# Optimization experiments

Hardware: AMD Instinct MI355X
Metric: run time of the kernel (lower is better)

## Reference

```python
import jax, jax.numpy as jnp
import numpy as np

B, L, W = 512, 16, 256


def setup_inputs() -> dict:
    key = jax.random.key(0)
    k = jax.random.split(key, 9)
    f32 = jnp.float32
    # spin configuration in {-1, +1}
    x = jax.random.randint(k[0], (B, L, L), 0, 2).astype(f32) * 2.0 - 1.0
    s = 1.0 / np.sqrt(W)
    W_ih = jax.random.normal(k[1], (3 * W, 2), f32) * s      # GRUCell input weights
    W_hh = jax.random.normal(k[2], (3 * W, W), f32) * s      # GRUCell hidden weights
    b_ih = jax.random.normal(k[3], (3 * W,), f32) * s
    b_hh = jax.random.normal(k[4], (3 * W,), f32) * s
    W_fc = jax.random.normal(k[5], (2, W), f32) * s          # fc1
    b_fc = jax.random.normal(k[6], (2,), f32) * s
    W_hcat = jax.random.normal(k[7], (W, 2 * W), f32) * (1.0 / np.sqrt(2 * W))  # intermediate_h
    W_xcat = jax.random.normal(k[8], (1, 2), f32) * 0.5      # intermediate_x
    return dict(x=x, W_ih=W_ih, W_hh=W_hh, b_ih=b_ih, b_hh=b_hh,
                W_fc=W_fc, b_fc=b_fc, W_hcat=W_hcat, W_xcat=W_xcat)


def _log_prob(x, W_ih, W_hh, b_ih, b_hh, W_fc, b_fc, W_hcat, W_xcat):
    Bsz, Ln, _ = x.shape
    Wd = W_hh.shape[1]
    mask = (1.0 + x) * 0.5                      # (1+x)/2
    Wh_l = W_hcat[:, :Wd]                       # acts on left-neighbor hidden (cat order: [left, up])
    Wh_u = W_hcat[:, Wd:]                       # acts on up-neighbor hidden

    def step(carry, xs):
        x_left, h_left = carry                  # [B], [B,W]
        x_cur, x_up, h_up, m = xs               # [B], [B], [B,W], [B]
        # intermediate_x(stack([x_left, x_up]))
        x_int = x_left * W_xcat[0, 0] + x_up * W_xcat[0, 1]
        # intermediate_h(cat([h_left, h_up]))
        h_int = h_left @ Wh_l.T + h_up @ Wh_u.T
        # embedded_x = [(x+1)/2, 1-(x+1)/2]
        p_up = (x_int + 1.0) * 0.5
        emb = jnp.stack([p_up, 1.0 - p_up], axis=1)   # [B,2]
        # torch.nn.GRUCell math (gate order: reset, update, new)
        gi = emb @ W_ih.T + b_ih
        gh = h_int @ W_hh.T + b_hh
        ir, iz, inn = jnp.split(gi, 3, axis=1)
        hr, hz, hn = jnp.split(gh, 3, axis=1)
        r = jax.nn.sigmoid(ir + hr)
        z = jax.nn.sigmoid(iz + hz)
        n = jnp.tanh(inn + r * hn)
        h_next = (1.0 - z) * n + z * h_int
        y = jax.nn.log_softmax(h_next @ W_fc.T + b_fc, axis=1)   # [B,2]
        lp = y[:, 0] * m + y[:, 1] * (1.0 - m)
        return (x_cur, h_next), (h_next, lp)

    h_prev = jnp.zeros((Ln, Bsz, Wd), x.dtype)  # hidden of row above, columns-major [L,B,W]
    x_prev = jnp.zeros((Ln, Bsz), x.dtype)      # spins of row above [L,B]
    lp_rows = []
    for i in range(Ln):                         # fixed small structural loop over rows
        x_row = x[:, i, :].T                    # [L,B]
        m_row = mask[:, i, :].T
        x_up, h_up = x_prev, h_prev
        if i % 2 == 1:                          # zigzag: odd rows scan right-to-left
            x_row, m_row = x_row[::-1], m_row[::-1]
            x_up, h_up = x_up[::-1], h_up[::-1]
        carry0 = (jnp.zeros((Bsz,), x.dtype), jnp.zeros((Bsz, Wd), x.dtype))
        _, (h_out, lp_out) = jax.lax.scan(step, carry0, (x_row, x_up, h_up, m_row))
        if i % 2 == 1:                          # restore grid (column) order
            h_out, lp_out = h_out[::-1], lp_out[::-1]
        lp_rows.append(lp_out)                  # [L,B]
        h_prev = h_out
        x_prev = x[:, i, :].T
    lp = jnp.transpose(jnp.stack(lp_rows, axis=0), (2, 0, 1))   # [B,L,L]
    lp = lp.at[:, 0, 0].set(1.0 - mask[:, 0, 0])                # first site overwrite
    return lp.sum(axis=(1, 2))


def reference(x, W_ih, W_hh, b_ih, b_hh, W_fc, b_fc, W_hcat, W_xcat):
    # z2 == 0 and reverse == False: log_prob(x) == _log_prob(x)
    return _log_prob(x, W_ih, W_hh, b_ih, b_hh, W_fc, b_fc, W_hcat, W_xcat)
```

## Files before the change

### kernel.cpp

```cpp
#include <hip/hip_runtime.h>
#include <math.h>

#define LL 16
#define WD 256
#define G3 768

#define OFF_AR  0
#define OFF_AL  36864
#define OFF_B8  65536
#define OFF_SR  114688
#define OFF_GA  115456
#define OFF_GBI 116224

typedef _Float16 h2v __attribute__((ext_vector_type(2)));

__device__ __forceinline__ unsigned packh2(float a, float b) {
    h2v v; v.x = (_Float16)a; v.y = (_Float16)b;
    return __builtin_bit_cast(unsigned, v);
}
__device__ __forceinline__ float dot2f(unsigned w, unsigned h, float acc) {
#if __has_builtin(__builtin_amdgcn_fdot2)
    return __builtin_amdgcn_fdot2(__builtin_bit_cast(h2v, w),
                                  __builtin_bit_cast(h2v, h), acc, false);
#else
    h2v a = __builtin_bit_cast(h2v, w), b = __builtin_bit_cast(h2v, h);
    return acc + (float)a.x * (float)b.x + (float)a.y * (float)b.y;
#endif
}
__device__ __forceinline__ int sdot4(unsigned a, unsigned b, int acc) {
#if __has_builtin(__builtin_amdgcn_sdot4)
    return __builtin_amdgcn_sdot4((int)a, (int)b, acc, false);
#else
    int s = acc;
    #pragma unroll
    for (int r = 0; r < 4; ++r)
        s += (int)(signed char)(a >> (8 * r)) * (int)(signed char)(b >> (8 * r));
    return s;
#endif
}
__device__ __forceinline__ unsigned short f16b(float v) {
    _Float16 h = (_Float16)v; return __builtin_bit_cast(unsigned short, h);
}
__device__ __forceinline__ float fsig(float v) { return 1.f / (1.f + __expf(-v)); }
__device__ __forceinline__ float ftanh_(float v) {
    v = fminf(fmaxf(v, -15.f), 15.f);
    float e = __expf(-2.f * v);
    return (1.f - e) / (1.f + e);
}
__device__ __forceinline__ int clampi8(int q) {
    return q > 127 ? 127 : (q < -127 ? -127 : q);
}

__global__ __launch_bounds__(64)
void gru2d_prep1(const float* __restrict__ W_hh, float* __restrict__ ws) {
    int row = blockIdx.x, lane = threadIdx.x;
    float s = 0.f;
    for (int k = lane; k < 256; k += 64) s = fmaxf(s, fabsf(W_hh[row * 256 + k]));
    #pragma unroll
    for (int o = 32; o > 0; o >>= 1) s = fmaxf(s, __shfl_down(s, o));
    if (lane == 0) ws[OFF_SR + row] = (s > 0.f) ? s * (1.f / 127.f) : 1.f;
}

__global__ __launch_bounds__(256)
void gru2d_prep2(const float* __restrict__ W_ih, const float* __restrict__ W_hh,
                 const float* __restrict__ b_ih, const float* __restrict__ W_hcat,
                 float* __restrict__ ws) {
    unsigned* __restrict__ wsu = (unsigned*)ws;
    int m = blockIdx.x * 256 + threadIdx.x;
    if (m < 36864) {
        int g = m >> 11, t5 = (m >> 2) & 511, r = m & 3;
        int w = t5 & 255, ch = t5 >> 8, j = g * 4 + r;
        int base = w * 512 + ch * 256 + 2 * j;
        wsu[OFF_AR + m] = packh2(W_hcat[base], W_hcat[base + 1]);
    } else if (m < 65536) {
        int mm = m - 36864;
        int g = mm >> 11, t5 = (mm >> 2) & 511, r = mm & 3;
        int w = t5 & 255, ch = t5 >> 8, j = 72 + g * 4 + r;
        int base = w * 512 + ch * 256 + 2 * j;
        wsu[OFF_AL + mm] = packh2(W_hcat[base], W_hcat[base + 1]);
    } else if (m < 114688) {
        int mm = m - 65536;
        int g4 = mm >> 11, t = (mm >> 2) & 511, rr = mm & 3;
        int ql = g4 * 4 + rr;
        int gate = ql >> 5, q = ql & 31;
        int v = t >> 6, l = t & 63;
        int wB_ = v * 32 + (l & 31), chB = l >> 5;
        int row = gate * 256 + wB_;
        float inv = 1.f / ws[OFF_SR + row];
        int kb = row * 256 + chB * 128 + 4 * q;
        unsigned pk = 0;
        #pragma unroll
        for (int bb = 0; bb < 4; ++bb) {
            int qv = clampi8(__float2int_rn(W_hh[kb + bb] * inv));
            pk |= ((unsigned)(qv & 255)) << (8 * bb);
        }
        wsu[OFF_B8 + mm] = pk;
    } else if (m < 115456) {
        int e = m - 114688;
        float w0 = W_ih[2 * e], w1 = W_ih[2 * e + 1];
        ws[OFF_GA + e] = w0 - w1;
        ws[OFF_GBI + e] = w1 + b_ih[e];
    }
}

__global__ __launch_bounds__(512, 2)
void gru2d_main(const float* __restrict__ x, const float* __restrict__ b_hh,
                const float* __restrict__ W_fc, const float* __restrict__ b_fc,
                const float* __restrict__ W_xcat, const float* __restrict__ ws,
                float* __restrict__ out) {
    __shared__ __attribute__((aligned(16))) uint4 ldsA[14 * 512];
    __shared__ __attribute__((aligned(16))) unsigned h2pk[2][128];
    __shared__ __attribute__((aligned(16))) unsigned hp2pk[2][LL][128];
    __shared__ __attribute__((aligned(16))) float pA[2][2][256];
    __shared__ __attribute__((aligned(16))) float shint[2][256];
    __shared__ __attribute__((aligned(16))) unsigned hint8[2][64];
    __shared__ float dqs[2][4];
    __shared__ float fcp[2][2][8];
    __shared__ float sx[2][256];

    const int tid = threadIdx.x;
    const int w = tid & 255;
    const int ch = tid >> 8;
    const int v = tid >> 6, l = tid & 63;
    const int lr = l & 31, sub = l >> 5;
    const int wB_ = (v << 5) + lr;
    const int b0 = blockIdx.x * 2;
    const unsigned* __restrict__ wsu = (const unsigned*)ws;

    unsigned wA[72], wB8[96];
    #pragma unroll
    for (int g = 0; g < 18; ++g) {
        uint4 q = ((const uint4*)(wsu + OFF_AR))[g * 512 + tid];
        wA[4*g] = q.x; wA[4*g+1] = q.y; wA[4*g+2] = q.z; wA[4*g+3] = q.w;
    }
    #pragma unroll
    for (int g = 0; g < 24; ++g) {
        uint4 q = ((const uint4*)(wsu + OFF_B8))[g * 512 + tid];
        wB8[4*g] = q.x; wB8[4*g+1] = q.y; wB8[4*g+2] = q.z; wB8[4*g+3] = q.w;
    }

    #pragma unroll
    for (int g = 0; g < 14; ++g)
        ldsA[g * 512 + tid] = ((const uint4*)(wsu + OFF_AL))[g * 512 + tid];
    float bA[3], bBi[3], bbh[3], bsr[3];
    #pragma unroll
    for (int g = 0; g < 3; ++g) {
        bA[g]  = ws[OFF_GA + (g << 8) + wB_];
        bBi[g] = ws[OFF_GBI + (g << 8) + wB_];
        bbh[g] = b_hh[(g << 8) + wB_];
        bsr[g] = ws[OFF_SR + (g << 8) + wB_];
    }
    const float wfc0 = W_fc[wB_], wfc1 = W_fc[256 + wB_];
    sx[ch][w] = x[(b0 + ch) * 256 + w];
    {
        unsigned* hp = (unsigned*)hp2pk;
        #pragma unroll
        for (int g = 0; g < 8; ++g) hp[g * 512 + tid] = 0u;
        if (tid < 256) ((unsigned*)h2pk)[tid] = 0u;
    }
    const float xc0 = W_xcat[0], xc1 = W_xcat[1];
    const float bf0 = b_fc[0], bf1 = b_fc[1];
    float lp_acc = 0.f;
    __syncthreads();

    for (int i = 0; i < LL; ++i) {
        const int odd = i & 1;
        const int dir = odd ? -1 : 1;
        const int c0g = odd ? (LL - 1) : 0;
        for (int t = 0; t < LL; ++t) {
            const int col = c0g + dir * t;
            const int sidx = (i << 4) + t;

            #pragma unroll
            for (int g = 0; g < 18; ++g)
                asm volatile("" : "+v"(wA[4*g]), "+v"(wA[4*g+1]), "+v"(wA[4*g+2]), "+v"(wA[4*g+3]));
            #pragma unroll
            for (int g = 0; g < 24; ++g)
                asm volatile("" : "+v"(wB8[4*g]), "+v"(wB8[4*g+1]), "+v"(wB8[4*g+2]), "+v"(wB8[4*g+3]));

            {
                const uint4* hb0;
                const uint4* hb1;
                if (ch == 0) {
                    hb0 = (const uint4*)h2pk;
                    hb1 = ((const uint4*)h2pk) + 32;
                } else {
                    hb0 = ((const uint4*)hp2pk) + (col << 5);
                    hb1 = ((const uint4*)hp2pk) + 512 + (col << 5);
                }
                float a0 = 0.f, c0 = 0.f, a1 = 0.f, c1 = 0.f;
                if (!(ch == 0 && t == 0)) {
                    #pragma unroll
                    for (int g = 0; g < 18; ++g) {
                        uint4 h0 = hb0[g], h1 = hb1[g];
                        a0 = dot2f(wA[4*g],   h0.x, a0); c0 = dot2f(wA[4*g+1], h0.y, c0);
                        a0 = dot2f(wA[4*g+2], h0.z, a0); c0 = dot2f(wA[4*g+3], h0.w, c0);
                        a1 = dot2f(wA[4*g],   h1.x, a1); c1 = dot2f(wA[4*g+1], h1.y, c1);
                        a1 = dot2f(wA[4*g+2], h1.z, a1); c1 = dot2f(wA[4*g+3], h1.w, c1);
                    }
                    #pragma unroll
                    for (int g = 0; g < 14; ++g) {
                        uint4 wa = ldsA[g * 512 + tid];
                        uint4 h0 = hb0[18 + g], h1 = hb1[18 + g];
                        a0 = dot2f(wa.x, h0.x, a0); c0 = dot2f(wa.y, h0.y, c0);
                        a0 = dot2f(wa.z, h0.z, a0); c0 = dot2f(wa.w, h0.w, c0);
                        a1 = dot2f(wa.x, h1.x, a1); c1 = dot2f(wa.y, h1.y, c1);
                        a1 = dot2f(wa.z, h1.z, a1); c1 = dot2f(wa.w, h1.w, c1);
                    }
                }
                pA[ch][0][w] = a0 + c0;
                pA[ch][1][w] = a1 + c1;
            }
            __syncthreads();

            {
                float hi = pA[0][ch][w] + pA[1][ch][w];
                shint[ch][w] = hi;
                float am = fabsf(hi);
                #pragma unroll
                for (int o = 1; o < 64; o <<= 1) am = fmaxf(am, __shfl_xor(am, o));
                float qsc = 127.f / fmaxf(am, 1e-20f);
                int q = clampi8(__float2int_rn(hi * qsc));
                ((unsigned char*)hint8)[(ch << 8) + w] = (unsigned char)(q & 255);
                if ((w & 63) == 0) dqs[ch][w >> 6] = am * (1.f / 127.f);

                if (w == 0 && sidx > 0) {
                    int ps = sidx - 1, pi2 = ps >> 4, pt2 = ps & 15;
                    int pcol = (pi2 & 1) ? (15 - pt2) : pt2;
                    float l0 = bf0, l1 = bf1;
                    #pragma unroll
                    for (int vv = 0; vv < 8; ++vv) { l0 += fcp[ch][0][vv]; l1 += fcp[ch][1][vv]; }
                    float mx = fmaxf(l0, l1);
                    float lse = mx + logf(__expf(l0 - mx) + __expf(l1 - mx));
                    float xcur = sx[ch][(pi2 << 4) + pcol];
                    float mm = (1.f + xcur) * 0.5f;
                    float lp = (l0 - lse) * mm + (l1 - lse) * (1.f - mm);
                    if (pi2 == 0 && pcol == 0) lp = 1.f - mm;
                    lp_acc += lp;
                }
            }
            __syncthreads();

            {
                const uint4* hq0 = ((const uint4*)hint8) + (sub << 3);
                const uint4* hq1 = ((const uint4*)hint8) + 16 + (sub << 3);
                int ra0=0,ra1=0,za0=0,za1=0,na0=0,na1=0;
                int rb0=0,rb1=0,zb0=0,zb1=0,nb0=0,nb1=0;
                #pragma unroll
                for (int gg = 0; gg < 4; ++gg) {
                    uint4 u0 = hq0[gg], u1 = hq1[gg];
                    const int k = gg << 2;
                    ra0 = sdot4(wB8[k],      u0.x, ra0); ra0 = sdot4(wB8[k+1],    u0.y, ra0);
                    ra0 = sdot4(wB8[k+2],    u0.z, ra0); ra0 = sdot4(wB8[k+3],    u0.w, ra0);
                    za0 = sdot4(wB8[32+k],   u0.x, za0); za0 = sdot4(wB8[32+k+1], u0.y, za0);
                    za0 = sdot4(wB8[32+k+2], u0.z, za0); za0 = sdot4(wB8[32+k+3], u0.w, za0);
                    na0 = sdot4(wB8[64+k],   u0.x, na0); na0 = sdot4(wB8[64+k+1], u0.y, na0);
                    na0 = sdot4(wB8[64+k+2], u0.z, na0); na0 = sdot4(wB8[64+k+3], u0.w, na0);
                    ra1 = sdot4(wB8[k],      u1.x, ra1); ra1 = sdot4(wB8[k+1],    u1.y, ra1);
                    ra1 = sdot4(wB8[k+2],    u1.z, ra1); ra1 = sdot4(wB8[k+3],    u1.w, ra1);
                    za1 = sdot4(wB8[32+k],   u1.x, za1); za1 = sdot4(wB8[32+k+1], u1.y, za1);
                    za1 = sdot4(wB8[32+k+2], u1.z, za1); za1 = sdot4(wB8[32+k+3], u1.w, za1);
                    na1 = sdot4(wB8[64+k],   u1.x, na1); na1 = sdot4(wB8[64+k+1], u1.y, na1);
                    na1 = sdot4(wB8[64+k+2], u1.z, na1); na1 = sdot4(wB8[64+k+3], u1.w, na1);
                }
                #pragma unroll
                for (int gg = 4; gg < 8; ++gg) {
                    uint4 u0 = hq0[gg], u1 = hq1[gg];
                    const int k = gg << 2;
                    rb0 = sdot4(wB8[k],      u0.x, rb0); rb0 = sdot4(wB8[k+1],    u0.y, rb0);
                    rb0 = sdot4(wB8[k+2],    u0.z, rb0); rb0 = sdot4(wB8[k+3],    u0.w, rb0);
                    zb0 = sdot4(wB8[32+k],   u0.x, zb0); zb0 = sdot4(wB8[32+k+1], u0.y, zb0);
                    zb0 = sdot4(wB8[32+k+2], u0.z, zb0); zb0 = sdot4(wB8[32+k+3], u0.w, zb0);
                    nb0 = sdot4(wB8[64+k],   u0.x, nb0); nb0 = sdot4(wB8[64+k+1], u0.y, nb0);
                    nb0 = sdot4(wB8[64+k+2], u0.z, nb0); nb0 = sdot4(wB8[64+k+3], u0.w, nb0);
                    rb1 = sdot4(wB8[k],      u1.x, rb1); rb1 = sdot4(wB8[k+1],    u1.y, rb1);
                    rb1 = sdot4(wB8[k+2],    u1.z, rb1); rb1 = sdot4(wB8[k+3],    u1.w, rb1);
                    zb1 = sdot4(wB8[32+k],   u1.x, zb1); zb1 = sdot4(wB8[32+k+1], u1.y, zb1);
                    zb1 = sdot4(wB8[32+k+2], u1.z, zb1); zb1 = sdot4(wB8[32+k+3], u1.w, zb1);
                    nb1 = sdot4(wB8[64+k],   u1.x, nb1); nb1 = sdot4(wB8[64+k+1], u1.y, nb1);
                    nb1 = sdot4(wB8[64+k+2], u1.z, nb1); nb1 = sdot4(wB8[64+k+3], u1.w, nb1);
                }
                const float d00 = dqs[0][2*sub], d01 = dqs[0][2*sub+1];
                const float d10 = dqs[1][2*sub], d11 = dqs[1][2*sub+1];
                float gr0 = (float)ra0 * d00 + (float)rb0 * d01;
                float gz0 = (float)za0 * d00 + (float)zb0 * d01;
                float gn0 = (float)na0 * d00 + (float)nb0 * d01;
                float gr1 = (float)ra1 * d10 + (float)rb1 * d11;
                float gz1 = (float)za1 * d10 + (float)zb1 * d11;
                float gn1 = (float)na1 * d10 + (float)nb1 * d11;
                gr0 += __shfl_xor(gr0, 32); gz0 += __shfl_xor(gz0, 32); gn0 += __shfl_xor(gn0, 32);
                gr1 += __shfl_xor(gr1, 32); gz1 += __shfl_xor(gz1, 32); gn1 += __shfl_xor(gn1, 32);

                const int bsel = sub;
                float GR = (bsel ? gr1 : gr0) * bsr[0];
                float GZ = (bsel ? gz1 : gz0) * bsr[1];
                float GN = (bsel ? gn1 : gn0) * bsr[2];
                float HI = shint[bsel][wB_];
                float xl = (t == 0) ? 0.f : sx[bsel][(i << 4) + col - dir];
                float xu = (i == 0) ? 0.f : sx[bsel][((i - 1) << 4) + col];
                float pu = (xl * xc0 + xu * xc1 + 1.f) * 0.5f;
                float rr_ = fsig(bA[0] * pu + bBi[0] + GR + bbh[0]);
                float zz = fsig(bA[1] * pu + bBi[1] + GZ + bbh[1]);
                float nn = ftanh_(bA[2] * pu + bBi[2] + rr_ * (GN + bbh[2]));
                float hn = (1.f - zz) * nn + zz * HI;
                unsigned short hu = f16b(hn);
                ((unsigned short*)h2pk)[(bsel << 8) + wB_] = hu;
                ((unsigned short*)hp2pk)[(bsel << 12) + (col << 8) + wB_] = hu;
                float s0 = hn * wfc0, s1 = hn * wfc1;
                #pragma unroll
                for (int o = 1; o < 32; o <<= 1) {
                    s0 += __shfl_xor(s0, o);
                    s1 += __shfl_xor(s1, o);
                }
                if (lr == 0) { fcp[bsel][0][v] = s0; fcp[bsel][1][v] = s1; }
            }
            __syncthreads();
        }
    }

    if (w == 0) {
        float l0 = bf0, l1 = bf1;
        #pragma unroll
        for (int vv = 0; vv < 8; ++vv) { l0 += fcp[ch][0][vv]; l1 += fcp[ch][1][vv]; }
        float mx = fmaxf(l0, l1);
        float lse = mx + logf(__expf(l0 - mx) + __expf(l1 - mx));
        float xcur = sx[ch][15 * 16 + 0];
        float mm = (1.f + xcur) * 0.5f;
        lp_acc += (l0 - lse) * mm + (l1 - lse) * (1.f - mm);
        out[b0 + ch] = lp_acc;
    }
}

extern "C" void kernel_launch(void* const* d_in, const int* in_sizes, int n_in,
                              void* d_out, int out_size, void* d_ws, size_t ws_size,
                              hipStream_t stream) {
    const float* x      = (const float*)d_in[0];
    const float* W_ih   = (const float*)d_in[1];
    const float* W_hh   = (const float*)d_in[2];
    const float* b_ih   = (const float*)d_in[3];
    const float* b_hh   = (const float*)d_in[4];
    const float* W_fc   = (const float*)d_in[5];
    const float* b_fc   = (const float*)d_in[6];
    const float* W_hcat = (const float*)d_in[7];
    const float* W_xcat = (const float*)d_in[8];
    float* out = (float*)d_out;
    float* ws  = (float*)d_ws;

    gru2d_prep1<<<768, 64, 0, stream>>>(W_hh, ws);
    gru2d_prep2<<<451, 256, 0, stream>>>(W_ih, W_hh, b_ih, W_hcat, ws);
    gru2d_main<<<256, 512, 0, stream>>>(x, b_hh, W_fc, b_fc, W_xcat, ws, out);
}
```

Before: 973.3 us.

## Quantize intermediate_h weights and hidden states to int8 with per-block scales

Replaces the fp16 packed W_hcat weights (split between registers and LDS) with int8 weights that have per-row scales and fit entirely in registers. Hidden states are now stored as int8 with per-32-element scales, computed through a wave max-reduction and shuffles. The first matvec uses sdot4 instead of fdot2, which cuts the LDS weight traffic and halves the hidden-state bytes read. In exchange it adds extra reductions and shuffles on the serial step path and loses precision.

```diff
diff --git a/kernel.cpp b/kernel.cpp
--- a/kernel.cpp
+++ b/kernel.cpp
@@ -5,28 +5,13 @@
 #define WD 256
 #define G3 768
 
-#define OFF_AR  0
-#define OFF_AL  36864
-#define OFF_B8  65536
-#define OFF_SR  114688
-#define OFF_GA  115456
-#define OFF_GBI 116224
-
-typedef _Float16 h2v __attribute__((ext_vector_type(2)));
-
-__device__ __forceinline__ unsigned packh2(float a, float b) {
-    h2v v; v.x = (_Float16)a; v.y = (_Float16)b;
-    return __builtin_bit_cast(unsigned, v);
-}
-__device__ __forceinline__ float dot2f(unsigned w, unsigned h, float acc) {
-#if __has_builtin(__builtin_amdgcn_fdot2)
-    return __builtin_amdgcn_fdot2(__builtin_bit_cast(h2v, w),
-                                  __builtin_bit_cast(h2v, h), acc, false);
-#else
-    h2v a = __builtin_bit_cast(h2v, w), b = __builtin_bit_cast(h2v, h);
-    return acc + (float)a.x * (float)b.x + (float)a.y * (float)b.y;
-#endif
-}
+#define OFF_A8  0
+#define OFF_B8  32768
+#define OFF_SRB 81920
+#define OFF_SRA 82688
+#define OFF_GA  82944
+#define OFF_GBI 83712
+
 __device__ __forceinline__ int sdot4(unsigned a, unsigned b, int acc) {
 #if __has_builtin(__builtin_amdgcn_sdot4)
     return __builtin_amdgcn_sdot4((int)a, (int)b, acc, false);
@@ -38,9 +23,6 @@
     return s;
 #endif
 }
-__device__ __forceinline__ unsigned short f16b(float v) {
-    _Float16 h = (_Float16)v; return __builtin_bit_cast(unsigned short, h);
-}
 __device__ __forceinline__ float fsig(float v) { return 1.f / (1.f + __expf(-v)); }
 __device__ __forceinline__ float ftanh_(float v) {
     v = fminf(fmaxf(v, -15.f), 15.f);
@@ -52,13 +34,23 @@
 }
 
 __global__ __launch_bounds__(64)
-void gru2d_prep1(const float* __restrict__ W_hh, float* __restrict__ ws) {
+void gru2d_prep1(const float* __restrict__ W_hh, const float* __restrict__ W_hcat,
+                 float* __restrict__ ws) {
     int row = blockIdx.x, lane = threadIdx.x;
     float s = 0.f;
-    for (int k = lane; k < 256; k += 64) s = fmaxf(s, fabsf(W_hh[row * 256 + k]));
+    if (row < 768) {
+        for (int k = lane; k < 256; k += 64) s = fmaxf(s, fabsf(W_hh[row * 256 + k]));
+    } else {
+        int r = row - 768;
+        for (int k = lane; k < 512; k += 64) s = fmaxf(s, fabsf(W_hcat[r * 512 + k]));
+    }
     #pragma unroll
     for (int o = 32; o > 0; o >>= 1) s = fmaxf(s, __shfl_down(s, o));
-    if (lane == 0) ws[OFF_SR + row] = (s > 0.f) ? s * (1.f / 127.f) : 1.f;
+    if (lane == 0) {
+        float sc = (s > 0.f) ? s * (1.f / 127.f) : 1.f;
+        if (row < 768) ws[OFF_SRB + row] = sc;
+        else           ws[OFF_SRA + (row - 768)] = sc;
+    }
 }
 
 __global__ __launch_bounds__(256)
@@ -67,26 +59,28 @@
                  float* __restrict__ ws) {
     unsigned* __restrict__ wsu = (unsigned*)ws;
     int m = blockIdx.x * 256 + threadIdx.x;
-    if (m < 36864) {
-        int g = m >> 11, t5 = (m >> 2) & 511, r = m & 3;
-        int w = t5 & 255, ch = t5 >> 8, j = g * 4 + r;
-        int base = w * 512 + ch * 256 + 2 * j;
-        wsu[OFF_AR + m] = packh2(W_hcat[base], W_hcat[base + 1]);
-    } else if (m < 65536) {
-        int mm = m - 36864;
-        int g = mm >> 11, t5 = (mm >> 2) & 511, r = mm & 3;
-        int w = t5 & 255, ch = t5 >> 8, j = 72 + g * 4 + r;
-        int base = w * 512 + ch * 256 + 2 * j;
-        wsu[OFF_AL + mm] = packh2(W_hcat[base], W_hcat[base + 1]);
-    } else if (m < 114688) {
-        int mm = m - 65536;
+    if (m < 32768) {
+        int g4 = m >> 11, t = (m >> 2) & 511, r = m & 3;
+        int j = g4 * 4 + r;
+        int w = t & 255, ch = t >> 8;
+        float inv = 1.f / ws[OFF_SRA + w];
+        int base = w * 512 + ch * 256 + 4 * j;
+        unsigned pk = 0;
+        #pragma unroll
+        for (int bb = 0; bb < 4; ++bb) {
+            int qv = clampi8(__float2int_rn(W_hcat[base + bb] * inv));
+            pk |= ((unsigned)(qv & 255)) << (8 * bb);
+        }
+        wsu[OFF_A8 + m] = pk;
+    } else if (m < 81920) {
+        int mm = m - 32768;
         int g4 = mm >> 11, t = (mm >> 2) & 511, rr = mm & 3;
         int ql = g4 * 4 + rr;
         int gate = ql >> 5, q = ql & 31;
         int v = t >> 6, l = t & 63;
         int wB_ = v * 32 + (l & 31), chB = l >> 5;
         int row = gate * 256 + wB_;
-        float inv = 1.f / ws[OFF_SR + row];
+        float inv = 1.f / ws[OFF_SRB + row];
         int kb = row * 256 + chB * 128 + 4 * q;
         unsigned pk = 0;
         #pragma unroll
@@ -95,8 +89,8 @@
             pk |= ((unsigned)(qv & 255)) << (8 * bb);
         }
         wsu[OFF_B8 + mm] = pk;
-    } else if (m < 115456) {
-        int e = m - 114688;
+    } else if (m < 82688) {
+        int e = m - 81920;
         float w0 = W_ih[2 * e], w1 = W_ih[2 * e + 1];
         ws[OFF_GA + e] = w0 - w1;
         ws[OFF_GBI + e] = w1 + b_ih[e];
@@ -108,12 +102,13 @@
                 const float* __restrict__ W_fc, const float* __restrict__ b_fc,
                 const float* __restrict__ W_xcat, const float* __restrict__ ws,
                 float* __restrict__ out) {
-    __shared__ __attribute__((aligned(16))) uint4 ldsA[14 * 512];
-    __shared__ __attribute__((aligned(16))) unsigned h2pk[2][128];
-    __shared__ __attribute__((aligned(16))) unsigned hp2pk[2][LL][128];
+    __shared__ __attribute__((aligned(16))) unsigned h8[2][64];
+    __shared__ __attribute__((aligned(16))) unsigned hp8[2][LL][64];
+    __shared__ float hs8[2][8];
+    __shared__ float hps8[2][LL][8];
     __shared__ __attribute__((aligned(16))) float pA[2][2][256];
     __shared__ __attribute__((aligned(16))) float shint[2][256];
-    __shared__ __attribute__((aligned(16))) unsigned hint8[2][64];
+    __shared__ __attribute__((aligned(16))) unsigned hint8q[2][64];
     __shared__ float dqs[2][4];
     __shared__ float fcp[2][2][8];
     __shared__ float sx[2][256];
@@ -127,11 +122,11 @@
     const int b0 = blockIdx.x * 2;
     const unsigned* __restrict__ wsu = (const unsigned*)ws;
 
-    unsigned wA[72], wB8[96];
-    #pragma unroll
-    for (int g = 0; g < 18; ++g) {
-        uint4 q = ((const uint4*)(wsu + OFF_AR))[g * 512 + tid];
-        wA[4*g] = q.x; wA[4*g+1] = q.y; wA[4*g+2] = q.z; wA[4*g+3] = q.w;
+    unsigned wA8[64], wB8[96];
+    #pragma unroll
+    for (int g = 0; g < 16; ++g) {
+        uint4 q = ((const uint4*)(wsu + OFF_A8))[g * 512 + tid];
+        wA8[4*g] = q.x; wA8[4*g+1] = q.y; wA8[4*g+2] = q.z; wA8[4*g+3] = q.w;
     }
     #pragma unroll
     for (int g = 0; g < 24; ++g) {
@@ -139,24 +134,22 @@
         wB8[4*g] = q.x; wB8[4*g+1] = q.y; wB8[4*g+2] = q.z; wB8[4*g+3] = q.w;
     }
 
-    #pragma unroll
-    for (int g = 0; g < 14; ++g)
-        ldsA[g * 512 + tid] = ((const uint4*)(wsu + OFF_AL))[g * 512 + tid];
+    const float ascale = ws[OFF_SRA + w];
     float bA[3], bBi[3], bbh[3], bsr[3];
     #pragma unroll
     for (int g = 0; g < 3; ++g) {
         bA[g]  = ws[OFF_GA + (g << 8) + wB_];
         bBi[g] = ws[OFF_GBI + (g << 8) + wB_];
         bbh[g] = b_hh[(g << 8) + wB_];
-        bsr[g] = ws[OFF_SR + (g << 8) + wB_];
+        bsr[g] = ws[OFF_SRB + (g << 8) + wB_];
     }
     const float wfc0 = W_fc[wB_], wfc1 = W_fc[256 + wB_];
     sx[ch][w] = x[(b0 + ch) * 256 + w];
     {
-        unsigned* hp = (unsigned*)hp2pk;
+        unsigned* hp = (unsigned*)hp8;
         #pragma unroll
-        for (int g = 0; g < 8; ++g) hp[g * 512 + tid] = 0u;
-        if (tid < 256) ((unsigned*)h2pk)[tid] = 0u;
+        for (int g = 0; g < 4; ++g) hp[g * 512 + tid] = 0u;
+        if (tid < 256) ((float*)hps8)[tid] = 0.f;
     }
     const float xc0 = W_xcat[0], xc1 = W_xcat[1];
     const float bf0 = b_fc[0], bf1 = b_fc[1];
@@ -172,44 +165,48 @@
             const int sidx = (i << 4) + t;
 
             #pragma unroll
-            for (int g = 0; g < 18; ++g)
-                asm volatile("" : "+v"(wA[4*g]), "+v"(wA[4*g+1]), "+v"(wA[4*g+2]), "+v"(wA[4*g+3]));
+            for (int g = 0; g < 16; ++g)
+                asm volatile("" : "+v"(wA8[4*g]), "+v"(wA8[4*g+1]), "+v"(wA8[4*g+2]), "+v"(wA8[4*g+3]));
             #pragma unroll
             for (int g = 0; g < 24; ++g)
                 asm volatile("" : "+v"(wB8[4*g]), "+v"(wB8[4*g+1]), "+v"(wB8[4*g+2]), "+v"(wB8[4*g+3]));
 
             {
-                const uint4* hb0;
-                const uint4* hb1;
+                const uint4* Hb0;
+                const uint4* Hb1;
+                const float* sc0;
+                const float* sc1;
                 if (ch == 0) {
-                    hb0 = (const uint4*)h2pk;
-                    hb1 = ((const uint4*)h2pk) + 32;
+                    Hb0 = (const uint4*)h8[0];       Hb1 = (const uint4*)h8[1];
+                    sc0 = hs8[0];                     sc1 = hs8[1];
                 } else {
-                    hb0 = ((const uint4*)hp2pk) + (col << 5);
-                    hb1 = ((const uint4*)hp2pk) + 512 + (col << 5);
-                }
-                float a0 = 0.f, c0 = 0.f, a1 = 0.f, c1 = 0.f;
+                    Hb0 = (const uint4*)hp8[0][col]; Hb1 = (const uint4*)hp8[1][col];
+                    sc0 = hps8[0][col];               sc1 = hps8[1][col];
+                }
+                float fa0 = 0.f, fa1 = 0.f;
                 if (!(ch == 0 && t == 0)) {
                     #pragma unroll
-                    for (int g = 0; g < 18; ++g) {
-                        uint4 h0 = hb0[g], h1 = hb1[g];
-                        a0 = dot2f(wA[4*g],   h0.x, a0); c0 = dot2f(wA[4*g+1], h0.y, c0);
-                        a0 = dot2f(wA[4*g+2], h0.z, a0); c0 = dot2f(wA[4*g+3], h0.w, c0);
-                        a1 = dot2f(wA[4*g],   h1.x, a1); c1 = dot2f(wA[4*g+1], h1.y, c1);
-                        a1 = dot2f(wA[4*g+2], h1.z, a1); c1 = dot2f(wA[4*g+3], h1.w, c1);
+                    for (int c = 0; c < 8; ++c) {
+                        uint4 u0a = Hb0[2*c], u0b = Hb0[2*c+1];
+                        uint4 u1a = Hb1[2*c], u1b = Hb1[2*c+1];
+                        int a0 = 0, a1 = 0;
+                        const int kk = c << 3;
+                        a0 = sdot4(wA8[kk],   u0a.x, a0); a0 = sdot4(wA8[kk+1], u0a.y, a0);
+                        a0 = sdot4(wA8[kk+2], u0a.z, a0); a0 = sdot4(wA8[kk+3], u0a.w, a0);
+                        a0 = sdot4(wA8[kk+4], u0b.x, a0); a0 = sdot4(wA8[kk+5], u0b.y, a0);
+                        a0 = sdot4(wA8[kk+6], u0b.z, a0); a0 = sdot4(wA8[kk+7], u0b.w, a0);
+                        a1 = sdot4(wA8[kk],   u1a.x, a1); a1 = sdot4(wA8[kk+1], u1a.y, a1);
+                        a1 = sdot4(wA8[kk+2], u1a.z, a1); a1 = sdot4(wA8[kk+3], u1a.w, a1);
+                        a1 = sdot4(wA8[kk+4], u1b.x, a1); a1 = sdot4(wA8[kk+5], u1b.y, a1);
+                        a1 = sdot4(wA8[kk+6], u1b.z, a1); a1 = sdot4(wA8[kk+7], u1b.w, a1);
+                        fa0 += (float)a0 * sc0[c];
+                        fa1 += (float)a1 * sc1[c];
                     }
-                    #pragma unroll
-                    for (int g = 0; g < 14; ++g) {
-                        uint4 wa = ldsA[g * 512 + tid];
-                        uint4 h0 = hb0[18 + g], h1 = hb1[18 + g];
-                        a0 = dot2f(wa.x, h0.x, a0); c0 = dot2f(wa.y, h0.y, c0);
-                        a0 = dot2f(wa.z, h0.z, a0); c0 = dot2f(wa.w, h0.w, c0);
-                        a1 = dot2f(wa.x, h1.x, a1); c1 = dot2f(wa.y, h1.y, c1);
-                        a1 = dot2f(wa.z, h1.z, a1); c1 = dot2f(wa.w, h1.w, c1);
-                    }
-                }
-                pA[ch][0][w] = a0 + c0;
-                pA[ch][1][w] = a1 + c1;
+                    fa0 *= ascale;
+                    fa1 *= ascale;
+                }
+                pA[ch][0][w] = fa0;
+                pA[ch][1][w] = fa1;
             }
             __syncthreads();
 
@@ -221,7 +218,7 @@
                 for (int o = 1; o < 64; o <<= 1) am = fmaxf(am, __shfl_xor(am, o));
                 float qsc = 127.f / fmaxf(am, 1e-20f);
                 int q = clampi8(__float2int_rn(hi * qsc));
-                ((unsigned char*)hint8)[(ch << 8) + w] = (unsigned char)(q & 255);
+                ((unsigned char*)hint8q)[(ch << 8) + w] = (unsigned char)(q & 255);
                 if ((w & 63) == 0) dqs[ch][w >> 6] = am * (1.f / 127.f);
 
                 if (w == 0 && sidx > 0) {
@@ -242,8 +239,8 @@
             __syncthreads();
 
             {
-                const uint4* hq0 = ((const uint4*)hint8) + (sub << 3);
-                const uint4* hq1 = ((const uint4*)hint8) + 16 + (sub << 3);
+                const uint4* hq0 = ((const uint4*)hint8q) + (sub << 3);
+                const uint4* hq1 = ((const uint4*)hint8q) + 16 + (sub << 3);
                 int ra0=0,ra1=0,za0=0,za1=0,na0=0,na1=0;
                 int rb0=0,rb1=0,zb0=0,zb1=0,nb0=0,nb1=0;
                 #pragma unroll
@@ -303,9 +300,27 @@
                 float zz = fsig(bA[1] * pu + bBi[1] + GZ + bbh[1]);
                 float nn = ftanh_(bA[2] * pu + bBi[2] + rr_ * (GN + bbh[2]));
                 float hn = (1.f - zz) * nn + zz * HI;
-                unsigned short hu = f16b(hn);
-                ((unsigned short*)h2pk)[(bsel << 8) + wB_] = hu;
-                ((unsigned short*)hp2pk)[(bsel << 12) + (col << 8) + wB_] = hu;
+
+                float am = fabsf(hn);
+                #pragma unroll
+                for (int o = 1; o < 32; o <<= 1) am = fmaxf(am, __shfl_xor(am, o));
+                float qs = 127.f / fmaxf(am, 1e-20f);
+                unsigned q = (unsigned)(clampi8(__float2int_rn(hn * qs)) & 255);
+                unsigned q1 = __shfl_down(q, 1);
+                unsigned q2 = __shfl_down(q, 2);
+                unsigned q3 = __shfl_down(q, 3);
+                if ((lr & 3) == 0) {
+                    unsigned pk = q | (q1 << 8) | (q2 << 16) | (q3 << 24);
+                    int idx = (v << 3) + (lr >> 2);
+                    h8[bsel][idx] = pk;
+                    hp8[bsel][col][idx] = pk;
+                }
+                if (lr == 0) {
+                    float hsc = am * (1.f / 127.f);
+                    hs8[bsel][v] = hsc;
+                    hps8[bsel][col][v] = hsc;
+                }
+
                 float s0 = hn * wfc0, s1 = hn * wfc1;
                 #pragma unroll
                 for (int o = 1; o < 32; o <<= 1) {
@@ -346,7 +361,7 @@
     float* out = (float*)d_out;
     float* ws  = (float*)d_ws;
 
-    gru2d_prep1<<<768, 64, 0, stream>>>(W_hh, ws);
-    gru2d_prep2<<<451, 256, 0, stream>>>(W_ih, W_hh, b_ih, W_hcat, ws);
+    gru2d_prep1<<<1024, 64, 0, stream>>>(W_hh, W_hcat, ws);
+    gru2d_prep2<<<323, 256, 0, stream>>>(W_ih, W_hh, b_ih, W_hcat, ws);
     gru2d_main<<<256, 512, 0, stream>>>(x, b_hh, W_fc, b_fc, W_xcat, ws, out);
 }
```

Measured after the change: 946.0 us. 2.8% less time.
